# Kernel optimization log

Hardware: AMD Instinct MI355X
Metric: run time of the kernel (lower is better)

The kernel has to match this reference:

```python
import jax, jax.numpy as jnp
import numpy as np
from jax import lax

D_MODEL = 512
D_STATE = 16
D_CONV = 4
EXPAND = 2
D_INNER = EXPAND * D_MODEL
DT_RANK = (D_MODEL + 15) // 16  # ceil(d_model/16) = 32
B = 2
L = 2048


def _silu(x):
    return x * jax.nn.sigmoid(x)


def _mamba_block(x, norm_w, norm_b, in_w, conv_w, conv_b, xproj_w, dt_w, dt_b, A_log, D_skip, out_w):
    # x: [B, L, D_MODEL]; pre-norm residual Mamba block.
    Bsz = x.shape[0]
    mu = x.mean(-1, keepdims=True)
    xc0 = x - mu
    xn = xc0 * lax.rsqrt((xc0 * xc0).mean(-1, keepdims=True) + 1e-5)
    xn = xn * norm_w + norm_b
    # in_proj (no bias): [B, L, 2*D_INNER]
    xz = jnp.einsum('bld,ed->ble', xn, in_w)
    xc, z = jnp.split(xz, 2, axis=-1)
    # depthwise causal conv over time
    xt = xc.transpose(0, 2, 1)  # [B, D_INNER, L]
    xt = lax.conv_general_dilated(xt, conv_w[:, None, :], (1,), [(D_CONV - 1, 0)],
                                  feature_group_count=D_INNER,
                                  dimension_numbers=('NCH', 'OIH', 'NCH'))
    xc = _silu((xt + conv_b[None, :, None]).transpose(0, 2, 1))  # [B, L, D_INNER]
    # x_proj -> (dt, B, C)
    dbc = jnp.einsum('bld,ed->ble', xc, xproj_w)
    dt, Bs, Cs = jnp.split(dbc, [DT_RANK, DT_RANK + D_STATE], axis=-1)
    delta = jax.nn.softplus(jnp.einsum('blr,dr->bld', dt, dt_w) + dt_b)  # [B, L, D_INNER]
    A = -jnp.exp(A_log)  # [D_INNER, D_STATE]

    def step(h, inp):
        d_t, B_t, C_t, u_t = inp  # [B,d], [B,n], [B,n], [B,d]
        h = jnp.exp(d_t[..., None] * A) * h + (d_t * u_t)[..., None] * B_t[:, None, :]
        y_t = jnp.einsum('bdn,bn->bd', h, C_t)
        return h, y_t

    xs = (delta.transpose(1, 0, 2), Bs.transpose(1, 0, 2), Cs.transpose(1, 0, 2), xc.transpose(1, 0, 2))
    h0 = jnp.zeros((Bsz, D_INNER, D_STATE), x.dtype)
    _, ys = lax.scan(step, h0, xs)
    y = ys.transpose(1, 0, 2) + xc * D_skip  # skip connection D*u
    y = y * _silu(z)
    return x + jnp.einsum('ble,de->bld', y, out_w)


def setup_inputs() -> dict:
    key = jax.random.key(0)
    ks = jax.random.split(key, 12)
    f = lambda k, shape, s=0.02: jax.random.normal(k, shape, jnp.float32) * s
    return {
        'v': jax.random.normal(ks[0], (B, L, D_MODEL), jnp.float32),
        'a': jax.random.normal(ks[1], (B, L, D_MODEL), jnp.float32),
        't': jax.random.normal(ks[2], (B, L, D_MODEL), jnp.float32),
        'norm_w': jnp.ones((3, D_MODEL), jnp.float32),
        'norm_b': jnp.zeros((3, D_MODEL), jnp.float32),
        'in_w': f(ks[3], (3, 2 * D_INNER, D_MODEL)),
        'conv_w': f(ks[4], (3, D_INNER, D_CONV), 0.1),
        'conv_b': jnp.zeros((3, D_INNER), jnp.float32),
        'xproj_w': f(ks[5], (3, DT_RANK + 2 * D_STATE, D_INNER)),
        'dt_w': f(ks[6], (3, D_INNER, DT_RANK), 0.1),
        'dt_b': jnp.full((3, D_INNER), -4.6, jnp.float32),  # softplus(-4.6) ~ 0.01
        'A_log': jnp.tile(jnp.log(jnp.arange(1, D_STATE + 1, dtype=jnp.float32)), (3, D_INNER, 1)),
        'D_skip': jnp.ones((3, D_INNER), jnp.float32),
        'out_w': f(ks[7], (3, D_MODEL, D_INNER)),
        'couple_w': f(ks[8], (3, D_MODEL, D_MODEL)),
        'coef': jnp.full((3,), 0.1, jnp.float32),  # alpha, beta, gamma
    }


def reference(v, a, t, norm_w, norm_b, in_w, conv_w, conv_b, xproj_w, dt_w, dt_b, A_log, D_skip, out_w, couple_w, coef):
    # cross-modal residual injection
    v_in = v + coef[0] * jnp.einsum('bld,ed->ble', a, couple_w[0])
    a_in = a + coef[1] * jnp.einsum('bld,ed->ble', t, couple_w[1])
    t_in = t + coef[2] * jnp.einsum('bld,ed->ble', v, couple_w[2])
    x = jnp.stack([v_in, a_in, t_in])  # [3, B, L, D]
    outs = jax.vmap(_mamba_block)(x, norm_w, norm_b, in_w, conv_w, conv_b, xproj_w,
                                  dt_w, dt_b, A_log, D_skip, out_w)
    return (outs[0], outs[1], outs[2])
```

## Files before the change

kernel.cpp:

```cpp
#include <hip/hip_runtime.h>
#include <hip/hip_bf16.h>

#define MODS 3
#define BSZ 2
#define LSEQ 2048
#define DMODEL 512
#define DINNER 1024
#define DTRANK 32
#define NSTATE 16
#define DCONV 4
#define MROWS (BSZ*LSEQ)
#define NCHUNK 64
#define CHUNK 32

#define LOG2E 1.44269504088896f
#define LN2   0.69314718055995f

typedef __attribute__((ext_vector_type(8))) short short8v;
typedef __attribute__((ext_vector_type(4))) short short4v;
typedef __attribute__((ext_vector_type(2))) short short2v;
typedef __attribute__((ext_vector_type(4))) float f32x4;

#if __has_builtin(__builtin_amdgcn_exp2f)
#define EXP2F __builtin_amdgcn_exp2f
#else
#define EXP2F exp2f
#endif
#if __has_builtin(__builtin_amdgcn_rcpf)
#define RCPF __builtin_amdgcn_rcpf
#else
#define RCPF(x) (1.0f / (x))
#endif

__device__ __forceinline__ short f2bf(float x) {
    __hip_bfloat16 h = __float2bfloat16(x);
    return __builtin_bit_cast(short, h);
}
__device__ __forceinline__ float bf2f(short s) {
    return __uint_as_float(((unsigned)(unsigned short)s) << 16);
}
__device__ __forceinline__ void gl_lds16(const short* g, short* l) {
    __builtin_amdgcn_global_load_lds(
        (const __attribute__((address_space(1))) unsigned int*)g,
        (__attribute__((address_space(3))) unsigned int*)l, 16, 0, 0);
}
__device__ __forceinline__ float sigmoid_f(float x) {
    return RCPF(1.f + EXP2F(-x * LOG2E));
}

template<int NJ, int BK>
__global__ __launch_bounds__(256) void gemm_bf16(
    const __hip_bfloat16* __restrict__ A_, const __hip_bfloat16* __restrict__ B_,
    int K, int lda, int ldb, long sA, long sB,
    float* __restrict__ Cf, __hip_bfloat16* __restrict__ Cb, int ldc, long sC,
    const float* __restrict__ res, long sRes,
    const float* __restrict__ resB, const float* __restrict__ resC,
    const float* __restrict__ coef_base, int coef_stride,
    const float* __restrict__ bias, long sBias, int act)
{
    constexpr int BN = NJ * 32;
    constexpr int ASZ = 128 * BK;
    constexpr int BSZe = BN * BK;
    __shared__ alignas(16) short As[2 * ASZ];
    __shared__ alignas(16) short Bs[2 * BSZe];
    const int z = blockIdx.z;
    const int bm0 = blockIdx.x * 128;
    const int bn0 = blockIdx.y * BN;
    const short* Ag = (const short*)A_ + z * sA + (long)bm0 * lda;
    const short* Bg = (const short*)B_ + z * sB + (long)bn0 * ldb;
    const int tid = threadIdx.x;
    const int lane = tid & 63;
    const int w = tid >> 6;
    const int wr = w >> 1, wc = w & 1;
    const int lr = lane & 15;
    const int sidx = lane >> 4;

    constexpr int SLOTS = BK / 8;
    const int srow = tid / SLOTS;
    const int sslot = tid % SLOTS;
    int swz;
    if constexpr (BK == 64) swz = srow & 7;
    else                    swz = (srow >> 1) & 3;
    const int sgcol = (sslot ^ swz) * 8;
    int fA;
    if constexpr (BK == 64) fA = lr & 7;
    else                    fA = (lr >> 1) & 3;

    constexpr int AINSTR = ASZ / 2048;
    constexpr int BINSTR = BSZe / 2048;
    constexpr int RPI = 2048 / BK;

    f32x4 acc[4][NJ];
    #pragma unroll
    for (int i = 0; i < 4; ++i)
        #pragma unroll
        for (int j = 0; j < NJ; ++j)
            acc[i][j] = (f32x4){0.f, 0.f, 0.f, 0.f};

    auto stage = [&](int buf, int k0) {
        #pragma unroll
        for (int i = 0; i < AINSTR; ++i)
            gl_lds16(Ag + (long)(i * RPI + srow) * lda + k0 + sgcol,
                     As + buf * ASZ + i * 2048 + tid * 8);
        #pragma unroll
        for (int i = 0; i < BINSTR; ++i)
            gl_lds16(Bg + (long)(i * RPI + srow) * ldb + k0 + sgcol,
                     Bs + buf * BSZe + i * 2048 + tid * 8);
    };
    auto compute = [&](int buf) {
        #pragma unroll
        for (int kh = 0; kh < BK / 32; ++kh) {
            const int sl = ((kh * 4 + sidx) ^ fA) * 8;
            short8v af[4], bfr[NJ];
            #pragma unroll
            for (int i = 0; i < 4; ++i)
                af[i] = *(const short8v*)&As[buf * ASZ + (wr * 64 + i * 16 + lr) * BK + sl];
            #pragma unroll
            for (int j = 0; j < NJ; ++j)
                bfr[j] = *(const short8v*)&Bs[buf * BSZe + (wc * NJ * 16 + j * 16 + lr) * BK + sl];
            #pragma unroll
            for (int i = 0; i < 4; ++i)
                #pragma unroll
                for (int j = 0; j < NJ; ++j)
                    acc[i][j] = __builtin_amdgcn_mfma_f32_16x16x32_bf16(af[i], bfr[j], acc[i][j], 0, 0, 0);
        }
    };

    stage(0, 0);
    __syncthreads();
    int cur = 0;
    for (int k0 = BK; k0 < K; k0 += BK) {
        stage(cur ^ 1, k0);
        compute(cur);
        __syncthreads();
        cur ^= 1;
    }
    compute(cur);

    const float alpha = coef_base ? coef_base[z * coef_stride] : 1.0f;
    const float* resz = nullptr;
    if (res) {
        if (resB) resz = (z == 0) ? res : ((z == 1) ? resB : resC);
        else      resz = res + z * sRes;
    }
    const float* biasz = bias ? bias + z * sBias : nullptr;
    float* Cfz = Cf ? Cf + (long)z * sC : nullptr;
    __hip_bfloat16* Cbz = Cb ? Cb + (long)z * sC : nullptr;
    #pragma unroll
    for (int i = 0; i < 4; ++i) {
        #pragma unroll
        for (int r = 0; r < 4; ++r) {
            const int row = bm0 + wr * 64 + i * 16 + (lane >> 4) * 4 + r;
            #pragma unroll
            for (int j = 0; j < NJ; ++j) {
                const int col = bn0 + wc * NJ * 16 + j * 16 + lr;
                float val = acc[i][j][r];
                if (biasz) val += biasz[col];
                if (act == 1)
                    val = (val > 20.f) ? val : LN2 * __log2f(1.f + EXP2F(val * LOG2E));
                val *= alpha;
                if (resz) val += resz[(long)row * ldc + col];
                if (Cfz) Cfz[(long)row * ldc + col] = val;
                else     Cbz[(long)row * ldc + col] = __float2bfloat16(val);
            }
        }
    }
}

__global__ __launch_bounds__(256) void prep_kernel(
    const float* __restrict__ a, const float* __restrict__ t, const float* __restrict__ v,
    __hip_bfloat16* __restrict__ sec_bf,
    const float* __restrict__ couple_w, __hip_bfloat16* __restrict__ cw_bf,
    const float* __restrict__ in_w, __hip_bfloat16* __restrict__ inw_bf,
    const float* __restrict__ xproj_w, __hip_bfloat16* __restrict__ xpw_bf,
    const float* __restrict__ dt_w, __hip_bfloat16* __restrict__ dtw_bf,
    const float* __restrict__ out_w, __hip_bfloat16* __restrict__ outw_bf,
    const float* __restrict__ conv_w, float* __restrict__ cwT,
    const float* __restrict__ A_log, float* __restrict__ A2T)
{
    long idx = (long)blockIdx.x * 256 + threadIdx.x;
    if (idx < 1572864) {
        const int m = (int)(idx >> 19);
        const long off = idx & 524287;
        const float* sec = (m == 0) ? a : (m == 1) ? t : v;
        float4 sv = ((const float4*)sec)[off];
        short4v s;
        s.x = f2bf(sv.x); s.y = f2bf(sv.y); s.z = f2bf(sv.z); s.w = f2bf(sv.w);
        ((short4v*)sec_bf)[idx] = s;
        return;
    }
    idx -= 1572864;
    if (idx < 1449984) {
        const float* s; __hip_bfloat16* d; long off = idx;
        if      (off < 196608)              { s = couple_w; d = cw_bf; }
        else if ((off -= 196608) < 786432)  { s = in_w;     d = inw_bf; }
        else if ((off -= 786432) < 49152)   { s = xproj_w;  d = xpw_bf; }
        else if ((off -= 49152) < 24576)    { s = dt_w;     d = dtw_bf; }
        else    { off -= 24576;               s = out_w;    d = outw_bf; }
        float4 vv = ((const float4*)s)[off];
        short4v o;
        o.x = f2bf(vv.x); o.y = f2bf(vv.y); o.z = f2bf(vv.z); o.w = f2bf(vv.w);
        ((short4v*)d)[off] = o;
        return;
    }
    idx -= 1449984;
    if (idx < 12288) {
        const int k = (int)(idx & 3);
        const int c = (int)((idx >> 2) & 1023);
        const int m = (int)(idx >> 12);
        cwT[(m * DCONV + k) * DINNER + c] = conv_w[idx];
        return;
    }
    idx -= 12288;
    if (idx < 49152) {
        const int c = (int)(idx & 1023);
        const int n = (int)((idx >> 10) & 15);
        const int m = (int)(idx >> 14);
        A2T[idx] = -EXP2F(A_log[((long)m * DINNER + c) * NSTATE + n] * LOG2E) * LOG2E;
    }
}

__global__ __launch_bounds__(256) void ln_kernel(const float* __restrict__ x, __hip_bfloat16* __restrict__ xn,
                                                 const float* __restrict__ nw, const float* __restrict__ nb)
{
    const int row = blockIdx.x;
    const int m = row >> 12;
    const int tid = threadIdx.x;
    const float2 v = *reinterpret_cast<const float2*>(x + (long)row * DMODEL + tid * 2);
    float s = v.x + v.y;
    float sq = v.x * v.x + v.y * v.y;
    #pragma unroll
    for (int off = 32; off > 0; off >>= 1) {
        s  += __shfl_down(s, off);
        sq += __shfl_down(sq, off);
    }
    __shared__ float ws_s[4], ws_q[4];
    const int wid = tid >> 6, lane = tid & 63;
    if (lane == 0) { ws_s[wid] = s; ws_q[wid] = sq; }
    __syncthreads();
    if (tid == 0) {
        float ts = ws_s[0] + ws_s[1] + ws_s[2] + ws_s[3];
        float tq = ws_q[0] + ws_q[1] + ws_q[2] + ws_q[3];
        float mu = ts / DMODEL;
        float var = tq / DMODEL - mu * mu;
        ws_s[0] = mu;
        ws_q[0] = rsqrtf(var + 1e-5f);
    }
    __syncthreads();
    const float mu = ws_s[0], rstd = ws_q[0];
    const int e0 = tid * 2;
    float2 w  = *reinterpret_cast<const float2*>(nw + m * DMODEL + e0);
    float2 bb = *reinterpret_cast<const float2*>(nb + m * DMODEL + e0);
    short2v o;
    o.x = f2bf((v.x - mu) * rstd * w.x + bb.x);
    o.y = f2bf((v.y - mu) * rstd * w.y + bb.y);
    *reinterpret_cast<short2v*>((short*)xn + (long)row * DMODEL + e0) = o;
}

__global__ __launch_bounds__(256) void conv_silu_kernel(const __hip_bfloat16* __restrict__ xz,
    const float* __restrict__ cwT, const float* __restrict__ cb, __hip_bfloat16* __restrict__ xc)
{
    const int idx = blockIdx.x * 256 + threadIdx.x;
    const int c8 = idx & 127;
    const int lt = (idx >> 7) & 255;
    const int mb = idx >> 15;
    const int m  = mb >> 1;
    const int c0 = c8 * 8;
    const int l0 = lt * 8;

    float4 wlo[DCONV], whi[DCONV];
    #pragma unroll
    for (int k = 0; k < DCONV; ++k) {
        wlo[k] = *(const float4*)&cwT[(m * DCONV + k) * DINNER + c0];
        whi[k] = *(const float4*)&cwT[(m * DCONV + k) * DINNER + c0 + 4];
    }
    const float4 blo = *(const float4*)&cb[m * DINNER + c0];
    const float4 bhi = *(const float4*)&cb[m * DINNER + c0 + 4];

    const short* base = (const short*)xz + (long)mb * LSEQ * 2048 + c0;
    short* obase = (short*)xc + (long)mb * LSEQ * DINNER + c0;

    short8v r0 = {}, r1 = {}, r2 = {};
    if (l0 - 3 >= 0) r0 = *(const short8v*)(base + (long)(l0 - 3) * 2048);
    if (l0 - 2 >= 0) r1 = *(const short8v*)(base + (long)(l0 - 2) * 2048);
    if (l0 - 1 >= 0) r2 = *(const short8v*)(base + (long)(l0 - 1) * 2048);

    #pragma unroll
    for (int i = 0; i < 8; ++i) {
        const short8v cur = *(const short8v*)(base + (long)(l0 + i) * 2048);
        float acc[8];
        #pragma unroll
        for (int j = 0; j < 4; ++j) {
            acc[j]     = ((const float*)&blo)[j];
            acc[4 + j] = ((const float*)&bhi)[j];
        }
        #pragma unroll
        for (int j = 0; j < 8; ++j) {
            const float w0 = (j < 4) ? ((const float*)&wlo[0])[j] : ((const float*)&whi[0])[j - 4];
            const float w1 = (j < 4) ? ((const float*)&wlo[1])[j] : ((const float*)&whi[1])[j - 4];
            const float w2 = (j < 4) ? ((const float*)&wlo[2])[j] : ((const float*)&whi[2])[j - 4];
            const float w3 = (j < 4) ? ((const float*)&wlo[3])[j] : ((const float*)&whi[3])[j - 4];
            acc[j] += w0 * bf2f(r0[j]) + w1 * bf2f(r1[j]) + w2 * bf2f(r2[j]) + w3 * bf2f(cur[j]);
        }
        short8v o;
        #pragma unroll
        for (int j = 0; j < 8; ++j)
            o[j] = f2bf(acc[j] * sigmoid_f(acc[j]));
        *(short8v*)(obase + (long)(l0 + i) * DINNER) = o;
        r0 = r1; r1 = r2; r2 = cur;
    }
}

__device__ __forceinline__ bool geo_check(const float* A2) {
    bool g = true;
    #pragma unroll
    for (int n = 1; n < NSTATE; ++n)
        g = g && (__builtin_fabsf(A2[n] - (float)(n + 1) * A2[0]) <= 1e-4f * __builtin_fabsf(A2[n]));
    return g;
}

__global__ __launch_bounds__(256) void scan_pass1_kernel(
    const __hip_bfloat16* __restrict__ delta, const __hip_bfloat16* __restrict__ xc,
    const __hip_bfloat16* __restrict__ dbc, const float* __restrict__ A2T,
    float* __restrict__ Fbuf, float* __restrict__ sumd)
{
    const int bx = blockIdx.x;
    const int chunk = bx & (NCHUNK - 1);
    const int cg = (bx >> 6) & 3;
    const int mb = bx >> 8;
    const int m = mb >> 1, b = mb & 1;
    const int tid = threadIdx.x;
    const int c = cg * 256 + tid;

    float A2[NSTATE];
    #pragma unroll
    for (int n = 0; n < NSTATE; ++n)
        A2[n] = A2T[((long)m * NSTATE + n) * DINNER + c];
    const bool geo = geo_check(A2);
    float h[NSTATE] = {};
    float sum_d = 0.f;

    __shared__ float sB[CHUNK][NSTATE];
    const short* dbc_mb = (const short*)dbc + (long)m * MROWS * 64 + (long)b * LSEQ * 64;
    const int t0 = chunk * CHUNK;
    for (int i = tid; i < CHUNK * NSTATE; i += 256) {
        int tt = i >> 4, j = i & 15;
        sB[tt][j] = bf2f(dbc_mb[(long)(t0 + tt) * 64 + 32 + j]);
    }
    __syncthreads();

    const short* dp = (const short*)delta;
    const short* up = (const short*)xc;
    const long base = ((long)mb * LSEQ + t0) * DINNER + c;
    if (geo) {
        #pragma unroll 4
        for (int tt = 0; tt < CHUNK; ++tt) {
            const float d = bf2f(dp[base + (long)tt * DINNER]);
            const float u = bf2f(up[base + (long)tt * DINNER]);
            const float du = d * u;
            sum_d += d;
            const float E = EXP2F(d * A2[0]);
            float e = 1.f;
            #pragma unroll
            for (int n = 0; n < NSTATE; ++n) {
                e *= E;
                h[n] = e * h[n] + du * sB[tt][n];
            }
        }
    } else {
        #pragma unroll 4
        for (int tt = 0; tt < CHUNK; ++tt) {
            const float d = bf2f(dp[base + (long)tt * DINNER]);
            const float u = bf2f(up[base + (long)tt * DINNER]);
            const float du = d * u;
            sum_d += d;
            #pragma unroll
            for (int n = 0; n < NSTATE; ++n) {
                float e = EXP2F(d * A2[n]);
                h[n] = e * h[n] + du * sB[tt][n];
            }
        }
    }
    const long ob = ((long)mb * NCHUNK + chunk) * (NSTATE * DINNER) + c;
    #pragma unroll
    for (int n = 0; n < NSTATE; ++n)
        Fbuf[ob + n * DINNER] = h[n];
    sumd[(((long)mb * NCHUNK + chunk) << 10) + c] = sum_d;
}

__global__ __launch_bounds__(256) void scan_pass2_kernel(float* __restrict__ Fbuf,
                                                         const float* __restrict__ sumd,
                                                         const float* __restrict__ A2T)
{
    const long idx = (long)blockIdx.x * 256 + threadIdx.x;
    const int mb = (int)(idx >> 14);
    const int cn = (int)(idx & 16383);
    const int n = cn >> 10;
    const int c = cn & 1023;
    const int m = mb >> 1;
    const float A2n = A2T[((long)m * NSTATE + n) * DINNER + c];
    float run = 0.f;
    #pragma unroll 4
    for (int k = 0; k < NCHUNK; ++k) {
        const long o = ((long)(mb * NCHUNK + k) << 14) + cn;
        const float f = Fbuf[o];
        const float p = EXP2F(sumd[(((long)mb * NCHUNK + k) << 10) + c] * A2n);
        Fbuf[o] = run;
        run = p * run + f;
    }
}

__global__ __launch_bounds__(256) void scan_pass3_kernel(
    const __hip_bfloat16* __restrict__ delta, const __hip_bfloat16* __restrict__ xc,
    const __hip_bfloat16* __restrict__ dbc, __hip_bfloat16* __restrict__ xz,
    const float* __restrict__ A2T, const float* __restrict__ D_skip,
    const float* __restrict__ Hin)
{
    const int bx = blockIdx.x;
    const int chunk = bx & (NCHUNK - 1);
    const int cg = (bx >> 6) & 3;
    const int mb = bx >> 8;
    const int m = mb >> 1, b = mb & 1;
    const int tid = threadIdx.x;
    const int c = cg * 256 + tid;

    float A2[NSTATE];
    #pragma unroll
    for (int n = 0; n < NSTATE; ++n)
        A2[n] = A2T[((long)m * NSTATE + n) * DINNER + c];
    const bool geo = geo_check(A2);
    const float Dsk = D_skip[m * DINNER + c];

    float h[NSTATE];
    const long ho = ((long)mb * NCHUNK + chunk) * (NSTATE * DINNER) + c;
    #pragma unroll
    for (int n = 0; n < NSTATE; ++n) h[n] = Hin[ho + n * DINNER];

    __shared__ float sBC[CHUNK][2 * NSTATE];
    const short* dbc_mb = (const short*)dbc + (long)m * MROWS * 64 + (long)b * LSEQ * 64;
    const int t0 = chunk * CHUNK;
    for (int i = tid; i < CHUNK * 2 * NSTATE; i += 256) {
        int tt = i >> 5, j = i & 31;
        sBC[tt][j] = bf2f(dbc_mb[(long)(t0 + tt) * 64 + 32 + j]);
    }
    __syncthreads();

    const short* dp = (const short*)delta;
    const short* up = (const short*)xc;
    short* xzp = (short*)xz;
    const long base = ((long)mb * LSEQ + t0) * DINNER + c;
    const long xbase = ((long)mb * LSEQ + t0) * 2048 + c;
    if (geo) {
        #pragma unroll 4
        for (int tt = 0; tt < CHUNK; ++tt) {
            const long idx = base + (long)tt * DINNER;
            const long xi  = xbase + (long)tt * 2048;
            const float d = bf2f(dp[idx]);
            const float u = bf2f(up[idx]);
            const float zv = bf2f(xzp[xi + 1024]);
            const float du = d * u;
            const float E = EXP2F(d * A2[0]);
            float e = 1.f;
            float y = 0.f;
            #pragma unroll
            for (int n = 0; n < NSTATE; ++n) {
                e *= E;
                h[n] = e * h[n] + du * sBC[tt][n];
                y += h[n] * sBC[tt][16 + n];
            }
            y += u * Dsk;
            xzp[xi] = f2bf(y * (zv * sigmoid_f(zv)));
        }
    } else {
        #pragma unroll 4
        for (int tt = 0; tt < CHUNK; ++tt) {
            const long idx = base + (long)tt * DINNER;
            const long xi  = xbase + (long)tt * 2048;
            const float d = bf2f(dp[idx]);
            const float u = bf2f(up[idx]);
            const float zv = bf2f(xzp[xi + 1024]);
            const float du = d * u;
            float y = 0.f;
            #pragma unroll
            for (int n = 0; n < NSTATE; ++n) {
                float e = EXP2F(d * A2[n]);
                h[n] = e * h[n] + du * sBC[tt][n];
                y += h[n] * sBC[tt][16 + n];
            }
            y += u * Dsk;
            xzp[xi] = f2bf(y * (zv * sigmoid_f(zv)));
        }
    }
}

extern "C" void kernel_launch(void* const* d_in, const int* in_sizes, int n_in,
                              void* d_out, int out_size, void* d_ws, size_t ws_size,
                              hipStream_t stream)
{
    const float* v       = (const float*)d_in[0];
    const float* a       = (const float*)d_in[1];
    const float* t       = (const float*)d_in[2];
    const float* norm_w  = (const float*)d_in[3];
    const float* norm_b  = (const float*)d_in[4];
    const float* in_w    = (const float*)d_in[5];
    const float* conv_w  = (const float*)d_in[6];
    const float* conv_b  = (const float*)d_in[7];
    const float* xproj_w = (const float*)d_in[8];
    const float* dt_w    = (const float*)d_in[9];
    const float* dt_b    = (const float*)d_in[10];
    const float* A_log   = (const float*)d_in[11];
    const float* D_skip  = (const float*)d_in[12];
    const float* out_w   = (const float*)d_in[13];
    const float* couple_w= (const float*)d_in[14];
    const float* coef    = (const float*)d_in[15];
    float* out = (float*)d_out;

    typedef __hip_bfloat16 bf;
    float* x_in   = (float*)d_ws;
    bf* xn_bf     = (bf*)(x_in + 6291456);
    bf* sec_bf    = xn_bf + 6291456;
    bf* xz_bf     = sec_bf + 6291456;
    bf* xc_bf     = xz_bf + 25165824;
    bf* delta_bf  = xc_bf + 12582912;
    bf* dbc_bf    = delta_bf + 12582912;
    bf* cw_bf     = dbc_bf + 786432;
    bf* inw_bf    = cw_bf + 786432;
    bf* xpw_bf    = inw_bf + 3145728;
    bf* dtw_bf    = xpw_bf + 196608;
    bf* outw_bf   = dtw_bf + 98304;
    float* cwT    = (float*)(outw_bf + 1572864);
    float* A2T    = cwT + 12288;
    float* Fbuf   = A2T + 49152;
    float* sumd   = Fbuf + 6291456;

    dim3 blk(256);

    prep_kernel<<<(1572864 + 1449984 + 12288 + 49152 + 255) / 256, blk, 0, stream>>>(
        a, t, v, sec_bf, couple_w, cw_bf, in_w, inw_bf, xproj_w, xpw_bf,
        dt_w, dtw_bf, out_w, outw_bf, conv_w, cwT, A_log, A2T);

    gemm_bf16<2, 32><<<dim3(32, 8, 3), blk, 0, stream>>>(
        sec_bf, cw_bf, 512, 512, 512, 2097152L, 262144L,
        x_in, nullptr, 512, 2097152L,
        v, 0L, a, t, coef, 1, nullptr, 0L, 0);
    ln_kernel<<<3*4096, blk, 0, stream>>>(x_in, xn_bf, norm_w, norm_b);
    gemm_bf16<4, 32><<<dim3(32, 16, 3), blk, 0, stream>>>(
        xn_bf, inw_bf, 512, 512, 512, 2097152L, 1048576L,
        nullptr, xz_bf, 2048, 8388608L, nullptr, 0L, nullptr, nullptr, nullptr, 0, nullptr, 0L, 0);
    conv_silu_kernel<<<768, blk, 0, stream>>>(xz_bf, cwT, conv_b, xc_bf);
    gemm_bf16<2, 32><<<dim3(32, 1, 3), blk, 0, stream>>>(
        xc_bf, xpw_bf, 1024, 1024, 1024, 4194304L, 65536L,
        nullptr, dbc_bf, 64, 262144L, nullptr, 0L, nullptr, nullptr, nullptr, 0, nullptr, 0L, 0);
    gemm_bf16<4, 32><<<dim3(32, 8, 3), blk, 0, stream>>>(
        dbc_bf, dtw_bf, 32, 64, 32, 262144L, 32768L,
        nullptr, delta_bf, 1024, 4194304L, nullptr, 0L, nullptr, nullptr, nullptr, 0, dt_b, 1024L, 1);
    scan_pass1_kernel<<<6*4*NCHUNK, blk, 0, stream>>>(delta_bf, xc_bf, dbc_bf, A2T, Fbuf, sumd);
    scan_pass2_kernel<<<(6*1024*16)/256, blk, 0, stream>>>(Fbuf, sumd, A2T);
    scan_pass3_kernel<<<6*4*NCHUNK, blk, 0, stream>>>(delta_bf, xc_bf, dbc_bf, xz_bf,
                                                      A2T, D_skip, Fbuf);
    gemm_bf16<2, 32><<<dim3(32, 8, 3), blk, 0, stream>>>(
        xz_bf, outw_bf, 1024, 2048, 1024, 8388608L, 524288L,
        out, nullptr, 512, 2097152L, x_in, 2097152L, nullptr, nullptr, nullptr, 0, nullptr, 0L, 0);
}
```

Measured before the change: 269.4 us.

## Replace in-proj GEMM with 256x256-tile 8-wave ping-pong bf16 kernel

Adds a dedicated in-projection GEMM that uses 256x256 output tiles, 512 threads (8 waves), BK=64 with XOR-swizzled LDS, and a quadrant-by-quadrant schedule. Global-to-LDS loads for the next K step are interleaved with MFMA work on the current one through explicit vmcnt waits and barriers. The aim is more data reuse per tile and better overlap of memory traffic with MFMA than the generic 128-row BK=32 kernel gives. The cost is heavy register pressure from 64 accumulator tiles per thread, a grid of only 384 blocks, and hand-written waitcnt counts that must stay exactly in step with the number of issued loads.

```diff
diff --git a/kernel.cpp b/kernel.cpp
--- a/kernel.cpp
+++ b/kernel.cpp
@@ -46,6 +46,140 @@
 }
 __device__ __forceinline__ float sigmoid_f(float x) {
     return RCPF(1.f + EXP2F(-x * LOG2E));
+}
+
+#define MFMAQ(QR, QC)                                                              \
+    _Pragma("unroll")                                                              \
+    for (int rf = 0; rf < 4; ++rf)                                                 \
+        _Pragma("unroll")                                                          \
+        for (int cf = 0; cf < 2; ++cf)                                             \
+            _Pragma("unroll")                                                      \
+            for (int kh = 0; kh < 2; ++kh)                                         \
+                acc[QR][QC][rf][cf] = __builtin_amdgcn_mfma_f32_16x16x32_bf16(     \
+                    afr[rf][kh], bfr[cf][kh], acc[QR][QC][rf][cf], 0, 0, 0);
+
+__global__ __launch_bounds__(512, 2) void gemm8p_inproj(
+    const __hip_bfloat16* __restrict__ A_, const __hip_bfloat16* __restrict__ B_,
+    __hip_bfloat16* __restrict__ C_)
+{
+    constexpr int NT = 8;
+    __shared__ alignas(16) short As[2 * 16384];
+    __shared__ alignas(16) short Bs[2 * 16384];
+    const int z = blockIdx.z;
+    const int bm0 = blockIdx.x * 256;
+    const int bn0 = blockIdx.y * 256;
+    const short* Ag = (const short*)A_ + (long)z * 2097152 + (long)bm0 * 512;
+    const short* Bg = (const short*)B_ + (long)z * 1048576 + (long)bn0 * 512;
+    short* Cg = (short*)C_ + (long)z * 8388608;
+    const int tid = threadIdx.x;
+    const int lane = tid & 63;
+    const int w = tid >> 6;
+    const int wr = w >> 2;
+    const int wc = w & 3;
+    const int lr = lane & 15;
+    const int sidx = lane >> 4;
+    const int srow_l = tid >> 3;
+    const int sgoff = ((tid & 7) ^ (srow_l & 7)) * 8;
+
+    f32x4 acc[2][2][4][2];
+    #pragma unroll
+    for (int a = 0; a < 2; ++a)
+        #pragma unroll
+        for (int b = 0; b < 2; ++b)
+            #pragma unroll
+            for (int c = 0; c < 4; ++c)
+                #pragma unroll
+                for (int d = 0; d < 2; ++d)
+                    acc[a][b][c][d] = (f32x4){0.f, 0.f, 0.f, 0.f};
+
+    short8v afr[4][2];
+    short8v bfr[2][2];
+
+    auto stageA = [&](int buf, int half, int t) {
+        #pragma unroll
+        for (int j = 0; j < 2; ++j) {
+            const int row = half * 128 + j * 64 + srow_l;
+            gl_lds16(Ag + (long)row * 512 + t * 64 + sgoff,
+                     As + buf * 16384 + half * 8192 + j * 4096 + tid * 8);
+        }
+    };
+    auto stageB = [&](int buf, int half, int t) {
+        #pragma unroll
+        for (int j = 0; j < 2; ++j) {
+            const int row = half * 128 + j * 64 + srow_l;
+            gl_lds16(Bg + (long)row * 512 + t * 64 + sgoff,
+                     Bs + buf * 16384 + half * 8192 + j * 4096 + tid * 8);
+        }
+    };
+    auto loadA = [&](int buf, int qr) {
+        #pragma unroll
+        for (int rf = 0; rf < 4; ++rf)
+            #pragma unroll
+            for (int kh = 0; kh < 2; ++kh) {
+                const int ra = qr * 128 + wr * 64 + rf * 16 + lr;
+                const int g = kh * 4 + sidx;
+                afr[rf][kh] = *(const short8v*)&As[buf * 16384 + ra * 64 + ((g ^ (ra & 7)) << 3)];
+            }
+    };
+    auto loadB = [&](int buf, int qc) {
+        #pragma unroll
+        for (int cf = 0; cf < 2; ++cf)
+            #pragma unroll
+            for (int kh = 0; kh < 2; ++kh) {
+                const int rb = qc * 128 + wc * 32 + cf * 16 + lr;
+                const int g = kh * 4 + sidx;
+                bfr[cf][kh] = *(const short8v*)&Bs[buf * 16384 + rb * 64 + ((g ^ (rb & 7)) << 3)];
+            }
+    };
+
+    stageA(0, 0, 0); stageB(0, 0, 0); stageA(0, 1, 0); stageB(0, 1, 0);
+
+    for (int t = 0; t < NT; ++t) {
+        const int p = t & 1;
+        const bool stg = (t + 1) < NT;
+        if (stg) { stageA(p ^ 1, 0, t + 1);
+                   asm volatile("s_waitcnt vmcnt(6)" ::: "memory"); }
+        else       asm volatile("s_waitcnt vmcnt(4)" ::: "memory");
+        asm volatile("s_barrier" ::: "memory");
+        loadA(p, 0); loadB(p, 0);
+        MFMAQ(0, 0)
+        asm volatile("s_barrier" ::: "memory");
+        if (stg) { stageB(p ^ 1, 0, t + 1);
+                   asm volatile("s_waitcnt vmcnt(6)" ::: "memory"); }
+        else       asm volatile("s_waitcnt vmcnt(2)" ::: "memory");
+        asm volatile("s_barrier" ::: "memory");
+        loadA(p, 1);
+        MFMAQ(1, 0)
+        asm volatile("s_barrier" ::: "memory");
+        if (stg) { stageA(p ^ 1, 1, t + 1);
+                   asm volatile("s_waitcnt vmcnt(6)" ::: "memory"); }
+        else       asm volatile("s_waitcnt vmcnt(0)" ::: "memory");
+        asm volatile("s_barrier" ::: "memory");
+        loadB(p, 1);
+        MFMAQ(1, 1)
+        asm volatile("s_barrier" ::: "memory");
+        if (stg) stageB(p ^ 1, 1, t + 1);
+        asm volatile("s_barrier" ::: "memory");
+        loadA(p, 0);
+        MFMAQ(0, 1)
+        asm volatile("s_barrier" ::: "memory");
+    }
+
+    #pragma unroll
+    for (int qr = 0; qr < 2; ++qr)
+        #pragma unroll
+        for (int qc = 0; qc < 2; ++qc)
+            #pragma unroll
+            for (int rf = 0; rf < 4; ++rf)
+                #pragma unroll
+                for (int r = 0; r < 4; ++r) {
+                    const int row = bm0 + qr * 128 + wr * 64 + rf * 16 + (lane >> 4) * 4 + r;
+                    #pragma unroll
+                    for (int cf = 0; cf < 2; ++cf) {
+                        const int col = bn0 + qc * 128 + wc * 32 + cf * 16 + lr;
+                        Cg[(long)row * 2048 + col] = f2bf(acc[qr][qc][rf][cf][r]);
+                    }
+                }
 }
 
 template<int NJ, int BK>
@@ -111,18 +245,18 @@
         #pragma unroll
         for (int kh = 0; kh < BK / 32; ++kh) {
             const int sl = ((kh * 4 + sidx) ^ fA) * 8;
-            short8v af[4], bfr[NJ];
+            short8v af[4], bfr2[NJ];
             #pragma unroll
             for (int i = 0; i < 4; ++i)
                 af[i] = *(const short8v*)&As[buf * ASZ + (wr * 64 + i * 16 + lr) * BK + sl];
             #pragma unroll
             for (int j = 0; j < NJ; ++j)
-                bfr[j] = *(const short8v*)&Bs[buf * BSZe + (wc * NJ * 16 + j * 16 + lr) * BK + sl];
+                bfr2[j] = *(const short8v*)&Bs[buf * BSZe + (wc * NJ * 16 + j * 16 + lr) * BK + sl];
             #pragma unroll
             for (int i = 0; i < 4; ++i)
                 #pragma unroll
                 for (int j = 0; j < NJ; ++j)
-                    acc[i][j] = __builtin_amdgcn_mfma_f32_16x16x32_bf16(af[i], bfr[j], acc[i][j], 0, 0, 0);
+                    acc[i][j] = __builtin_amdgcn_mfma_f32_16x16x32_bf16(af[i], bfr2[j], acc[i][j], 0, 0, 0);
         }
     };
 
@@ -544,9 +678,7 @@
         x_in, nullptr, 512, 2097152L,
         v, 0L, a, t, coef, 1, nullptr, 0L, 0);
     ln_kernel<<<3*4096, blk, 0, stream>>>(x_in, xn_bf, norm_w, norm_b);
-    gemm_bf16<4, 32><<<dim3(32, 16, 3), blk, 0, stream>>>(
-        xn_bf, inw_bf, 512, 512, 512, 2097152L, 1048576L,
-        nullptr, xz_bf, 2048, 8388608L, nullptr, 0L, nullptr, nullptr, nullptr, 0, nullptr, 0L, 0);
+    gemm8p_inproj<<<dim3(16, 8, 3), 512, 0, stream>>>(xn_bf, inw_bf, xz_bf);
     conv_silu_kernel<<<768, blk, 0, stream>>>(xz_bf, cwT, conv_b, xc_bf);
     gemm_bf16<2, 32><<<dim3(32, 1, 3), blk, 0, stream>>>(
         xc_bf, xpw_bf, 1024, 1024, 1024, 4194304L, 65536L,
```

Measured after the change: 259.9 us. -3.5%, faster.
